# Optimization experiments

Hardware: AMD Instinct MI355X
Metric: run time of the kernel (lower is better)

The kernel has to match this reference:

```python
import jax, jax.numpy as jnp
import numpy as np

DIM = 512
HEADS = 8        # MultiHeadAttention default heads=8 (init 'heads' arg actually sets dim_head)
DIM_HEAD = 64    # from AttentionLayers heads=64 passed positionally as dim_head
HIDDEN = HEADS * DIM_HEAD  # 512
EPS = 1e-5


def setup_inputs() -> dict:
    key = jax.random.key(0)
    ks = jax.random.split(key, 8)
    s = 1.0 / np.sqrt(DIM)
    return {
        "x": jax.random.normal(ks[0], (4, 2048, DIM), dtype=jnp.float32),
        "ln_g": jnp.ones((DIM,), dtype=jnp.float32),
        "ln_b": jnp.zeros((DIM,), dtype=jnp.float32),
        "Wq": jax.random.normal(ks[1], (DIM, HIDDEN), dtype=jnp.float32) * s,
        "Wk": jax.random.normal(ks[2], (DIM, HIDDEN), dtype=jnp.float32) * s,
        "Wv": jax.random.normal(ks[3], (DIM, HIDDEN), dtype=jnp.float32) * s,
        "Wo": jax.random.normal(ks[4], (HIDDEN, DIM), dtype=jnp.float32) * s,
        "bo": jnp.zeros((DIM,), dtype=jnp.float32),
    }


def reference(x, ln_g, ln_b, Wq, Wk, Wv, Wo, bo):
    b, n, d = x.shape
    residual = x
    # pre-norm LayerNorm
    mu = jnp.mean(x, axis=-1, keepdims=True)
    var = jnp.mean((x - mu) ** 2, axis=-1, keepdims=True)
    xn = (x - mu) * jax.lax.rsqrt(var + EPS) * ln_g + ln_b
    # QKV projections (no bias), split into heads: [b, s, h, dh]
    q = (xn @ Wq).reshape(b, n, HEADS, DIM_HEAD)
    k = (xn @ Wk).reshape(b, n, HEADS, DIM_HEAD)
    v = (xn @ Wv).reshape(b, n, HEADS, DIM_HEAD)
    scale = HIDDEN ** (-0.5)  # note: scales by hidden_dim, not dim_head (faithful)
    scores = jnp.einsum('bihd,bjhd->bhij', q, k) * scale  # [b,h,i,j] full matrix
    attn = jax.nn.softmax(scores, axis=-1)
    out = jnp.einsum('bhij,bjhd->bihd', attn, v).reshape(b, n, HIDDEN)
    out = out @ Wo + bo
    # residual; the subsequent FFN layer's output is discarded in the source
    return out + residual
```

## Files before the change

kernel.cpp:

```cpp
#include <hip/hip_runtime.h>
#include <hip/hip_bf16.h>

#define DIM 512
#define SEQ 2048
#define BATCH 4
#define NHEADS 8
#define DH 64
#define NROWS (BATCH * SEQ)
#define LN_EPS 1e-5f

typedef __hip_bfloat16 bf16;
typedef __attribute__((ext_vector_type(8))) short short8;
typedef __attribute__((ext_vector_type(4))) float f32x4;
typedef __attribute__((ext_vector_type(16))) float f32x16;

#define MFMA16(a, b, c) __builtin_amdgcn_mfma_f32_16x16x32_bf16((a), (b), (c), 0, 0, 0)
#define MFMA32(a, b, c) __builtin_amdgcn_mfma_f32_32x32x16_bf16((a), (b), (c), 0, 0, 0)

#if __has_builtin(__builtin_amdgcn_exp2f)
#define EXP2(x) __builtin_amdgcn_exp2f(x)
#else
#define EXP2(x) exp2f(x)
#endif

#if defined(__has_builtin)
#if __has_builtin(__builtin_amdgcn_global_load_lds)
#define HAS_GLDS 1
#endif
#endif

__device__ __forceinline__ void glds16(const bf16* g, bf16* l) {
#ifdef HAS_GLDS
  __builtin_amdgcn_global_load_lds((const __attribute__((address_space(1))) void*)g,
                                   (__attribute__((address_space(3))) void*)l, 16, 0, 0);
#else
  *reinterpret_cast<uint4*>(l) = *reinterpret_cast<const uint4*>(g);
#endif
}

__device__ __forceinline__ void store_bf16x4(bf16* p, float a, float b, float c, float d) {
  bf16 tmp[4] = {__float2bfloat16(a), __float2bfloat16(b), __float2bfloat16(c),
                 __float2bfloat16(d)};
  *reinterpret_cast<ushort4*>(p) = *reinterpret_cast<const ushort4*>(tmp);
}

__device__ __forceinline__ unsigned pk2(float a, float b) {
  union { bf16 h[2]; unsigned u; } x;
  x.h[0] = __float2bfloat16(a);
  x.h[1] = __float2bfloat16(b);
  return x.u;
}

__device__ __forceinline__ short8 mk8(unsigned a, unsigned b, unsigned c, unsigned d) {
  union { unsigned u[4]; short8 s; } x;
  x.u[0] = a; x.u[1] = b; x.u[2] = c; x.u[3] = d;
  return x.s;
}

#define B2F(us) __uint_as_float(((unsigned)(us)) << 16)

#define BARRIER() asm volatile("s_barrier" ::: "memory")
#define WAITVM0() asm volatile("s_waitcnt vmcnt(0)" ::: "memory")

#define Q_SCALE_LOG2E 0.06375872f

__global__ void setup_kernel(const float* __restrict__ x, const float* __restrict__ gamma,
                             const float* __restrict__ beta, bf16* __restrict__ xn,
                             const float* __restrict__ Wq, const float* __restrict__ Wk,
                             const float* __restrict__ Wv, const float* __restrict__ Wo,
                             bf16* __restrict__ Wt) {
  const int t = threadIdx.x;
  if (blockIdx.x < NROWS / 4) {
    const int row = blockIdx.x * 4 + (t >> 6);
    const int l = t & 63;
    const float4* xr = reinterpret_cast<const float4*>(x + (size_t)row * DIM);
    const float4 v0 = xr[l * 2];
    const float4 v1 = xr[l * 2 + 1];
    float s = (v0.x + v0.y + v0.z + v0.w) + (v1.x + v1.y + v1.z + v1.w);
    float ss = v0.x * v0.x + v0.y * v0.y + v0.z * v0.z + v0.w * v0.w + v1.x * v1.x +
               v1.y * v1.y + v1.z * v1.z + v1.w * v1.w;
#pragma unroll
    for (int off = 1; off < 64; off <<= 1) {
      s += __shfl_xor(s, off);
      ss += __shfl_xor(ss, off);
    }
    const float mu = s * (1.0f / DIM);
    const float rs = rsqrtf(ss * (1.0f / DIM) - mu * mu + LN_EPS);
    const float4 g0 = reinterpret_cast<const float4*>(gamma)[l * 2];
    const float4 g1 = reinterpret_cast<const float4*>(gamma)[l * 2 + 1];
    const float4 b0 = reinterpret_cast<const float4*>(beta)[l * 2];
    const float4 b1 = reinterpret_cast<const float4*>(beta)[l * 2 + 1];
    bf16* o = xn + (size_t)row * DIM + l * 8;
    store_bf16x4(o, (v0.x - mu) * rs * g0.x + b0.x, (v0.y - mu) * rs * g0.y + b0.y,
                 (v0.z - mu) * rs * g0.z + b0.z, (v0.w - mu) * rs * g0.w + b0.w);
    store_bf16x4(o + 4, (v1.x - mu) * rs * g1.x + b1.x, (v1.y - mu) * rs * g1.y + b1.y,
                 (v1.z - mu) * rs * g1.z + b1.z, (v1.w - mu) * rs * g1.w + b1.w);
  } else {
    __shared__ float tile[32][33];
    const int idx = blockIdx.x - NROWS / 4;
    const int bx = idx & 15, by = (idx >> 4) & 15, z = idx >> 8;
    const float* __restrict__ W = (z == 0) ? Wq : (z == 1) ? Wk : (z == 2) ? Wv : Wo;
    const float scale = (z == 0) ? Q_SCALE_LOG2E : 1.0f;
    bf16* __restrict__ dst = Wt + (size_t)z * DIM * DIM;
    const int tx = t & 31, ty = t >> 5;
#pragma unroll
    for (int i = 0; i < 32; i += 8)
      tile[ty + i][tx] = W[(size_t)(by * 32 + ty + i) * DIM + bx * 32 + tx];
    __syncthreads();
#pragma unroll
    for (int i = 0; i < 32; i += 8)
      dst[(size_t)(bx * 32 + ty + i) * DIM + by * 32 + tx] =
          __float2bfloat16(tile[tx][ty + i] * scale);
  }
}

__launch_bounds__(256, 3)
__global__ void gemm_qkv_kernel(const bf16* __restrict__ A, const bf16* __restrict__ Bt,
                                bf16* __restrict__ qo, bf16* __restrict__ ko,
                                bf16* __restrict__ vto) {
  const int m0 = blockIdx.x * 128, n0g = blockIdx.y * 128;
  __shared__ __align__(16) char smem[128 * 136 * 2];
  bf16* const sA = (bf16*)smem;
  bf16* const sB = (bf16*)(smem + 16384);
  bf16* const sT = (bf16*)smem;
  const int t = threadIdx.x, w = t >> 6, l = t & 63;
  const int r = l & 15, g = l >> 4;
  const int wm = w >> 1, wn = w & 1;
  const int crow = w * 32 + (l >> 2);
  const int ccol = (l & 3) * 8;
  const bf16* gA = A + (size_t)(m0 + crow) * DIM + ccol;
  const bf16* gB = Bt + (size_t)(n0g + crow) * DIM + ccol;
  const int loff = w * 1024 + l * 8;
  f32x4 acc[4][4] = {};
  glds16(gA, sA + loff);
  glds16(gA + 16 * DIM, sA + loff + 512);
  glds16(gB, sB + loff);
  glds16(gB + 16 * DIM, sB + loff + 512);
  const int NK = DIM / 32;
  for (int ks = 0; ks < NK; ks++) {
    const int cur = ks & 1;
    __syncthreads();
    if (ks + 1 < NK) {
      const int k0n = (ks + 1) * 32;
      glds16(gA + k0n, sA + (1 - cur) * 4096 + loff);
      glds16(gA + 16 * DIM + k0n, sA + (1 - cur) * 4096 + loff + 512);
      glds16(gB + k0n, sB + (1 - cur) * 4096 + loff);
      glds16(gB + 16 * DIM + k0n, sB + (1 - cur) * 4096 + loff + 512);
    }
    short8 af[4], bfv[4];
#pragma unroll
    for (int i = 0; i < 4; i++)
      af[i] = *reinterpret_cast<const short8*>(
          &sA[cur * 4096 + (wm * 64 + i * 16 + r) * 32 + g * 8]);
#pragma unroll
    for (int j = 0; j < 4; j++)
      bfv[j] = *reinterpret_cast<const short8*>(
          &sB[cur * 4096 + (wn * 64 + j * 16 + r) * 32 + g * 8]);
#pragma unroll
    for (int i = 0; i < 4; i++)
#pragma unroll
      for (int j = 0; j < 4; j++) acc[i][j] = MFMA16(af[i], bfv[j], acc[i][j]);
  }
  const int z = n0g >> 9;
  const int b = m0 / SEQ;
  if (z != 2) {
    bf16* __restrict__ outp = (z == 0) ? qo : ko;
    const int nc0 = (n0g & 511) + wn * 64;
#pragma unroll
    for (int i = 0; i < 4; i++)
#pragma unroll
      for (int j = 0; j < 4; j++)
#pragma unroll
        for (int reg = 0; reg < 4; reg++) {
          const int m = m0 + wm * 64 + i * 16 + g * 4 + reg;
          const int col = nc0 + j * 16 + r;
          outp[(size_t)m * DIM + col] = __float2bfloat16(acc[i][j][reg]);
        }
  } else {
    __syncthreads();
#pragma unroll
    for (int i = 0; i < 4; i++)
#pragma unroll
      for (int j = 0; j < 4; j++)
        store_bf16x4(&sT[(wn * 64 + j * 16 + r) * 136 + wm * 64 + i * 16 + g * 4],
                     acc[i][j][0], acc[i][j][1], acc[i][j][2], acc[i][j][3]);
    __syncthreads();
    const int dr = t >> 1;
    const int mc = (t & 1) * 64;
    const int dcol = (n0g & 511) + dr;
    bf16* dst = vto + ((size_t)b * DIM + dcol) * SEQ + (m0 - b * SEQ) + mc;
#pragma unroll
    for (int uu = 0; uu < 8; uu++)
      *reinterpret_cast<uint4*>(dst + uu * 8) =
          *reinterpret_cast<const uint4*>(&sT[dr * 136 + mc + uu * 8]);
  }
}

template <bool SPLIT>
__launch_bounds__(256, 2)
__global__ void attn_kernel(const bf16* __restrict__ q, const bf16* __restrict__ k,
                            const bf16* __restrict__ vt, bf16* __restrict__ opart,
                            float* __restrict__ lpart) {
  const int bh = blockIdx.x, jh = blockIdx.y, it = blockIdx.z;
  const int b = bh >> 3, h = bh & 7;
  const int t = threadIdx.x, wv = t >> 6, l = t & 63;
  const int c2 = l & 31, h2 = l >> 5;
  __shared__ __align__(16) bf16 sK[2][64 * 64];
  __shared__ __align__(16) bf16 sV[2][64 * 64];
  const int i0w = it * 256 + wv * 64;
  const int jbase = SPLIT ? jh * (SEQ / 2) : 0;

  const int srow8 = l >> 3;
  const int u = ((l & 7) - srow8) & 7;
  const bf16* kg = k + ((size_t)(b * SEQ) + jbase + wv * 16 + srow8) * DIM + h * DH + u * 8;
  const bf16* vg = vt + ((size_t)(b * DIM) + h * DH + wv * 16 + srow8) * SEQ + jbase + u * 8;
  const int loff = wv * 1024 + l * 8;
#pragma unroll
  for (int cc = 0; cc < 2; cc++) {
    glds16(kg + (size_t)(cc * 8) * DIM, &sK[0][loff + cc * 512]);
    glds16(vg + (size_t)(cc * 8) * SEQ, &sV[0][loff + cc * 512]);
  }

  const bf16* qp = q + ((size_t)(b * SEQ) + i0w + c2) * DIM + h * DH + h2 * 8;
  short8 qf[2][4];
#pragma unroll
  for (int x = 0; x < 2; x++)
#pragma unroll
    for (int kk = 0; kk < 4; kk++)
      qf[x][kk] = *reinterpret_cast<const short8*>(qp + x * 32 * DIM + kk * 16);

  int eo[4];
#pragma unroll
  for (int x = 0; x < 4; x++) eo[x] = c2 * 64 + 8 * ((2 * x + h2 + c2) & 7);

  f32x16 oacc[2][2] = {};
  float lsum[2] = {0.f, 0.f};
  const int NJ = SPLIT ? (SEQ / 2) / 64 : SEQ / 64;

  for (int jt = 0; jt < NJ; jt++) {
    WAITVM0();
    BARRIER();
    if (jt + 1 < NJ) {
      const int j0n = (jt + 1) * 64;
      const int bn = (jt + 1) & 1;
#pragma unroll
      for (int cc = 0; cc < 2; cc++) {
        glds16(kg + (size_t)(j0n + cc * 8) * DIM, &sK[bn][loff + cc * 512]);
        glds16(vg + (size_t)(cc * 8) * SEQ + j0n, &sV[bn][loff + cc * 512]);
      }
    }
    const bf16* sKb = sK[jt & 1];
    const bf16* sVb = sV[jt & 1];
#pragma unroll
    for (int jb = 0; jb < 2; jb++) {
      short8 kf[4];
#pragma unroll
      for (int kk = 0; kk < 4; kk++)
        kf[kk] = *reinterpret_cast<const short8*>(sKb + jb * 2048 + eo[kk]);
      f32x16 st[2] = {};
#pragma unroll
      for (int kk = 0; kk < 4; kk++) {
        st[0] = MFMA32(kf[kk], qf[0][kk], st[0]);
        st[1] = MFMA32(kf[kk], qf[1][kk], st[1]);
      }
      short8 pf[2][2];
#pragma unroll
      for (int x = 0; x < 2; x++) {
        float p[16];
#pragma unroll
        for (int e = 0; e < 16; e++) p[e] = EXP2(st[x][e]);
        lsum[x] += ((((p[0] + p[1]) + (p[2] + p[3])) + ((p[4] + p[5]) + (p[6] + p[7]))) +
                    (((p[8] + p[9]) + (p[10] + p[11])) + ((p[12] + p[13]) + (p[14] + p[15]))));
        unsigned W[4][2];
#pragma unroll
        for (int a = 0; a < 4; a++)
#pragma unroll
          for (int w = 0; w < 2; w++) W[a][w] = pk2(p[4 * a + 2 * w], p[4 * a + 2 * w + 1]);
#pragma unroll
        for (int k2 = 0; k2 < 2; k2++) {
          unsigned F0, F1, F2, F3;
          {
            const unsigned We = W[2 * k2][0], Wo = W[2 * k2 + 1][0];
            const unsigned te = __shfl_xor(We, 32), to = __shfl_xor(Wo, 32);
            F0 = h2 ? to : We;
            F2 = h2 ? Wo : te;
          }
          {
            const unsigned We = W[2 * k2][1], Wo = W[2 * k2 + 1][1];
            const unsigned te = __shfl_xor(We, 32), to = __shfl_xor(Wo, 32);
            F1 = h2 ? to : We;
            F3 = h2 ? Wo : te;
          }
          pf[x][k2] = mk8(F0, F1, F2, F3);
        }
      }
#pragma unroll
      for (int j2 = 0; j2 < 2; j2++) {
#pragma unroll
        for (int db = 0; db < 2; db++) {
          const short8 vf =
              *reinterpret_cast<const short8*>(sVb + db * 2048 + eo[2 * jb + j2]);
          oacc[0][db] = MFMA32(vf, pf[0][j2], oacc[0][db]);
          oacc[1][db] = MFMA32(vf, pf[1][j2], oacc[1][db]);
        }
      }
    }
  }
  const size_t obase = ((size_t)(SPLIT ? jh * 32 : 0) + bh) * SEQ;
#pragma unroll
  for (int x = 0; x < 2; x++) {
    lsum[x] += __shfl_xor(lsum[x], 32);
    const int i = i0w + x * 32 + c2;
    if (l < 32) lpart[obase + i] = lsum[x];
#pragma unroll
    for (int db = 0; db < 2; db++)
#pragma unroll
      for (int rr = 0; rr < 4; rr++)
        store_bf16x4(opart + (obase + i) * 64 + db * 32 + rr * 8 + h2 * 4,
                     oacc[x][db][4 * rr + 0], oacc[x][db][4 * rr + 1],
                     oacc[x][db][4 * rr + 2], oacc[x][db][4 * rr + 3]);
  }
  if (!SPLIT) {
    const size_t obase1 = ((size_t)32 + bh) * SEQ;
#pragma unroll
    for (int x = 0; x < 2; x++) {
      const int i = i0w + x * 32 + c2;
      if (l < 32) lpart[obase1 + i] = 0.f;
#pragma unroll
      for (int db = 0; db < 2; db++)
#pragma unroll
        for (int rr = 0; rr < 4; rr++)
          store_bf16x4(opart + (obase1 + i) * 64 + db * 32 + rr * 8 + h2 * 4, 0.f, 0.f, 0.f,
                       0.f);
    }
  }
}

__launch_bounds__(256, 2)
__global__ void gemm_proj_kernel(const bf16* __restrict__ opart, const float* __restrict__ lpart,
                                 const bf16* __restrict__ Bt, const float* __restrict__ bo,
                                 const float* __restrict__ x, float* __restrict__ out) {
  const int m0 = blockIdx.x * 128, n0 = blockIdx.y * 64;
  __shared__ __align__(16) bf16 sA[128 * 32];
  __shared__ __align__(16) bf16 sB[64 * 32];
  const int t = threadIdx.x, w = t >> 6, l = t & 63;
  const int r = l & 15, g = l >> 4;
  const int wm = w >> 1, wn = w & 1;
  const int arow = t >> 2;
  const int acol = (t & 3) * 8;
  const bf16* gB = Bt + (size_t)(n0 + arow) * DIM + acol;
  f32x4 acc[4][2] = {};
  const int NK = DIM / 32;
  for (int ks = 0; ks < NK; ks++) {
    const int k0 = ks * 32;
    const int h = k0 >> 6;
    const int d0 = (k0 & 63) + acol;
    uint4 areg[2];
#pragma unroll
    for (int c = 0; c < 2; c++) {
      const int m = m0 + c * 64 + arow;
      const int bb = m >> 11, ii = m & 2047;
      const size_t row0 = ((size_t)(bb * 8 + h)) * SEQ + ii;
      const size_t row1 = row0 + (size_t)32 * SEQ;
      const uint4 A0 = *reinterpret_cast<const uint4*>(opart + row0 * 64 + d0);
      const uint4 A1 = *reinterpret_cast<const uint4*>(opart + row1 * 64 + d0);
      const float inv = 1.0f / (lpart[row0] + lpart[row1]);
      const ushort* a0 = (const ushort*)&A0;
      const ushort* a1 = (const ushort*)&A1;
      bf16 rr[8];
#pragma unroll
      for (int e = 0; e < 8; e++)
        rr[e] = __float2bfloat16((B2F(a0[e]) + B2F(a1[e])) * inv);
      areg[c] = *reinterpret_cast<const uint4*>(rr);
    }
    const uint4 breg = *reinterpret_cast<const uint4*>(gB + k0);
    __syncthreads();
    *reinterpret_cast<uint4*>(&sA[(0 * 64 + arow) * 32 + acol]) = areg[0];
    *reinterpret_cast<uint4*>(&sA[(1 * 64 + arow) * 32 + acol]) = areg[1];
    *reinterpret_cast<uint4*>(&sB[arow * 32 + acol]) = breg;
    __syncthreads();
    short8 af[4], bfv[2];
#pragma unroll
    for (int i = 0; i < 4; i++)
      af[i] = *reinterpret_cast<const short8*>(&sA[(wm * 64 + i * 16 + r) * 32 + g * 8]);
#pragma unroll
    for (int j = 0; j < 2; j++)
      bfv[j] = *reinterpret_cast<const short8*>(&sB[(wn * 32 + j * 16 + r) * 32 + g * 8]);
#pragma unroll
    for (int i = 0; i < 4; i++)
#pragma unroll
      for (int j = 0; j < 2; j++) acc[i][j] = MFMA16(af[i], bfv[j], acc[i][j]);
  }
#pragma unroll
  for (int i = 0; i < 4; i++)
#pragma unroll
    for (int j = 0; j < 2; j++)
#pragma unroll
      for (int reg = 0; reg < 4; reg++) {
        const int m = m0 + wm * 64 + i * 16 + g * 4 + reg;
        const int col = n0 + wn * 32 + j * 16 + r;
        out[(size_t)m * DIM + col] = acc[i][j][reg] + bo[col] + x[(size_t)m * DIM + col];
      }
}

extern "C" void kernel_launch(void* const* d_in, const int* in_sizes, int n_in,
                              void* d_out, int out_size, void* d_ws, size_t ws_size,
                              hipStream_t stream) {
  (void)in_sizes; (void)n_in; (void)out_size;
  const float* x    = (const float*)d_in[0];
  const float* ln_g = (const float*)d_in[1];
  const float* ln_b = (const float*)d_in[2];
  const float* Wq   = (const float*)d_in[3];
  const float* Wk   = (const float*)d_in[4];
  const float* Wv   = (const float*)d_in[5];
  const float* Wo   = (const float*)d_in[6];
  const float* bo   = (const float*)d_in[7];
  float* out = (float*)d_out;
  char* ws = (char*)d_ws;
  bf16* xn  = (bf16*)(ws);
  bf16* wt  = (bf16*)(ws + (8u << 20));
  bf16* qb  = (bf16*)(ws + (10u << 20));
  bf16* kb  = (bf16*)(ws + (18u << 20));
  bf16* vtb = (bf16*)(ws + (26u << 20));
  bf16* opart = (bf16*)(ws + (34u << 20));
  float* lpart = (float*)(ws + (50u << 20));
  const bool split = ws_size >= ((50u << 20) + (1u << 19));

  setup_kernel<<<NROWS / 4 + 1024, 256, 0, stream>>>(x, ln_g, ln_b, xn, Wq, Wk, Wv, Wo, wt);
  gemm_qkv_kernel<<<dim3(NROWS / 128, (3 * DIM) / 128), 256, 0, stream>>>(xn, wt, qb, kb, vtb);
  if (split) {
    attn_kernel<true><<<dim3(BATCH * NHEADS, 2, SEQ / 256), 256, 0, stream>>>(
        qb, kb, vtb, opart, lpart);
  } else {
    attn_kernel<false><<<dim3(BATCH * NHEADS, 1, SEQ / 256), 256, 0, stream>>>(
        qb, kb, vtb, opart, lpart);
  }
  gemm_proj_kernel<<<dim3(NROWS / 128, DIM / 64), 256, 0, stream>>>(
      opart, lpart, wt + 3 * DIM * DIM, bo, x, out);
}
```

Before: 170.0 us.

## Halve per-wave query rows in attention to double blocks and occupancy

The attention kernel now gives each wave 32 query rows instead of 64, so a block covers 128 rows and the grid doubles along the sequence. The register footprint drops (one score tile, half the accumulators), and launch bounds are raised to 4 blocks per SIMD to match. The intent is more parallelism and better latency hiding. The cost is that every K/V tile loaded into LDS is reused by half as many query rows, which doubles K/V global and LDS traffic.

```diff
diff --git a/kernel.cpp b/kernel.cpp
--- a/kernel.cpp
+++ b/kernel.cpp
@@ -197,7 +197,7 @@
 }
 
 template <bool SPLIT>
-__launch_bounds__(256, 2)
+__launch_bounds__(256, 4)
 __global__ void attn_kernel(const bf16* __restrict__ q, const bf16* __restrict__ k,
                             const bf16* __restrict__ vt, bf16* __restrict__ opart,
                             float* __restrict__ lpart) {
@@ -207,7 +207,7 @@
   const int c2 = l & 31, h2 = l >> 5;
   __shared__ __align__(16) bf16 sK[2][64 * 64];
   __shared__ __align__(16) bf16 sV[2][64 * 64];
-  const int i0w = it * 256 + wv * 64;
+  const int i0w = it * 128 + wv * 32;
   const int jbase = SPLIT ? jh * (SEQ / 2) : 0;
 
   const int srow8 = l >> 3;
@@ -222,19 +222,17 @@
   }
 
   const bf16* qp = q + ((size_t)(b * SEQ) + i0w + c2) * DIM + h * DH + h2 * 8;
-  short8 qf[2][4];
-#pragma unroll
-  for (int x = 0; x < 2; x++)
-#pragma unroll
-    for (int kk = 0; kk < 4; kk++)
-      qf[x][kk] = *reinterpret_cast<const short8*>(qp + x * 32 * DIM + kk * 16);
+  short8 qf[4];
+#pragma unroll
+  for (int kk = 0; kk < 4; kk++)
+    qf[kk] = *reinterpret_cast<const short8*>(qp + kk * 16);
 
   int eo[4];
 #pragma unroll
   for (int x = 0; x < 4; x++) eo[x] = c2 * 64 + 8 * ((2 * x + h2 + c2) & 7);
 
-  f32x16 oacc[2][2] = {};
-  float lsum[2] = {0.f, 0.f};
+  f32x16 oacc[2] = {};
+  float lsum = 0.f;
   const int NJ = SPLIT ? (SEQ / 2) / 64 : SEQ / 64;
 
   for (int jt = 0; jt < NJ; jt++) {
@@ -257,42 +255,36 @@
 #pragma unroll
       for (int kk = 0; kk < 4; kk++)
         kf[kk] = *reinterpret_cast<const short8*>(sKb + jb * 2048 + eo[kk]);
-      f32x16 st[2] = {};
-#pragma unroll
-      for (int kk = 0; kk < 4; kk++) {
-        st[0] = MFMA32(kf[kk], qf[0][kk], st[0]);
-        st[1] = MFMA32(kf[kk], qf[1][kk], st[1]);
-      }
-      short8 pf[2][2];
-#pragma unroll
-      for (int x = 0; x < 2; x++) {
-        float p[16];
-#pragma unroll
-        for (int e = 0; e < 16; e++) p[e] = EXP2(st[x][e]);
-        lsum[x] += ((((p[0] + p[1]) + (p[2] + p[3])) + ((p[4] + p[5]) + (p[6] + p[7]))) +
-                    (((p[8] + p[9]) + (p[10] + p[11])) + ((p[12] + p[13]) + (p[14] + p[15]))));
-        unsigned W[4][2];
-#pragma unroll
-        for (int a = 0; a < 4; a++)
-#pragma unroll
-          for (int w = 0; w < 2; w++) W[a][w] = pk2(p[4 * a + 2 * w], p[4 * a + 2 * w + 1]);
-#pragma unroll
-        for (int k2 = 0; k2 < 2; k2++) {
-          unsigned F0, F1, F2, F3;
-          {
-            const unsigned We = W[2 * k2][0], Wo = W[2 * k2 + 1][0];
-            const unsigned te = __shfl_xor(We, 32), to = __shfl_xor(Wo, 32);
-            F0 = h2 ? to : We;
-            F2 = h2 ? Wo : te;
-          }
-          {
-            const unsigned We = W[2 * k2][1], Wo = W[2 * k2 + 1][1];
-            const unsigned te = __shfl_xor(We, 32), to = __shfl_xor(Wo, 32);
-            F1 = h2 ? to : We;
-            F3 = h2 ? Wo : te;
-          }
-          pf[x][k2] = mk8(F0, F1, F2, F3);
+      f32x16 st = {};
+#pragma unroll
+      for (int kk = 0; kk < 4; kk++) st = MFMA32(kf[kk], qf[kk], st);
+      float p[16];
+#pragma unroll
+      for (int e = 0; e < 16; e++) p[e] = EXP2(st[e]);
+      lsum += ((((p[0] + p[1]) + (p[2] + p[3])) + ((p[4] + p[5]) + (p[6] + p[7]))) +
+               (((p[8] + p[9]) + (p[10] + p[11])) + ((p[12] + p[13]) + (p[14] + p[15]))));
+      unsigned W[4][2];
+#pragma unroll
+      for (int a = 0; a < 4; a++)
+#pragma unroll
+        for (int w = 0; w < 2; w++) W[a][w] = pk2(p[4 * a + 2 * w], p[4 * a + 2 * w + 1]);
+      short8 pf[2];
+#pragma unroll
+      for (int k2 = 0; k2 < 2; k2++) {
+        unsigned F0, F1, F2, F3;
+        {
+          const unsigned We = W[2 * k2][0], Wo = W[2 * k2 + 1][0];
+          const unsigned te = __shfl_xor(We, 32), to = __shfl_xor(Wo, 32);
+          F0 = h2 ? to : We;
+          F2 = h2 ? Wo : te;
         }
+        {
+          const unsigned We = W[2 * k2][1], Wo = W[2 * k2 + 1][1];
+          const unsigned te = __shfl_xor(We, 32), to = __shfl_xor(Wo, 32);
+          F1 = h2 ? to : We;
+          F3 = h2 ? Wo : te;
+        }
+        pf[k2] = mk8(F0, F1, F2, F3);
       }
 #pragma unroll
       for (int j2 = 0; j2 < 2; j2++) {
@@ -300,39 +292,31 @@
         for (int db = 0; db < 2; db++) {
           const short8 vf =
               *reinterpret_cast<const short8*>(sVb + db * 2048 + eo[2 * jb + j2]);
-          oacc[0][db] = MFMA32(vf, pf[0][j2], oacc[0][db]);
-          oacc[1][db] = MFMA32(vf, pf[1][j2], oacc[1][db]);
+          oacc[db] = MFMA32(vf, pf[j2], oacc[db]);
         }
       }
     }
   }
   const size_t obase = ((size_t)(SPLIT ? jh * 32 : 0) + bh) * SEQ;
-#pragma unroll
-  for (int x = 0; x < 2; x++) {
-    lsum[x] += __shfl_xor(lsum[x], 32);
-    const int i = i0w + x * 32 + c2;
-    if (l < 32) lpart[obase + i] = lsum[x];
-#pragma unroll
-    for (int db = 0; db < 2; db++)
-#pragma unroll
-      for (int rr = 0; rr < 4; rr++)
-        store_bf16x4(opart + (obase + i) * 64 + db * 32 + rr * 8 + h2 * 4,
-                     oacc[x][db][4 * rr + 0], oacc[x][db][4 * rr + 1],
-                     oacc[x][db][4 * rr + 2], oacc[x][db][4 * rr + 3]);
-  }
+  lsum += __shfl_xor(lsum, 32);
+  const int i = i0w + c2;
+  if (l < 32) lpart[obase + i] = lsum;
+#pragma unroll
+  for (int db = 0; db < 2; db++)
+#pragma unroll
+    for (int rr = 0; rr < 4; rr++)
+      store_bf16x4(opart + (obase + i) * 64 + db * 32 + rr * 8 + h2 * 4,
+                   oacc[db][4 * rr + 0], oacc[db][4 * rr + 1], oacc[db][4 * rr + 2],
+                   oacc[db][4 * rr + 3]);
   if (!SPLIT) {
     const size_t obase1 = ((size_t)32 + bh) * SEQ;
-#pragma unroll
-    for (int x = 0; x < 2; x++) {
-      const int i = i0w + x * 32 + c2;
-      if (l < 32) lpart[obase1 + i] = 0.f;
-#pragma unroll
-      for (int db = 0; db < 2; db++)
-#pragma unroll
-        for (int rr = 0; rr < 4; rr++)
-          store_bf16x4(opart + (obase1 + i) * 64 + db * 32 + rr * 8 + h2 * 4, 0.f, 0.f, 0.f,
-                       0.f);
-    }
+    if (l < 32) lpart[obase1 + i] = 0.f;
+#pragma unroll
+    for (int db = 0; db < 2; db++)
+#pragma unroll
+      for (int rr = 0; rr < 4; rr++)
+        store_bf16x4(opart + (obase1 + i) * 64 + db * 32 + rr * 8 + h2 * 4, 0.f, 0.f, 0.f,
+                     0.f);
   }
 }
 
@@ -429,10 +413,10 @@
   setup_kernel<<<NROWS / 4 + 1024, 256, 0, stream>>>(x, ln_g, ln_b, xn, Wq, Wk, Wv, Wo, wt);
   gemm_qkv_kernel<<<dim3(NROWS / 128, (3 * DIM) / 128), 256, 0, stream>>>(xn, wt, qb, kb, vtb);
   if (split) {
-    attn_kernel<true><<<dim3(BATCH * NHEADS, 2, SEQ / 256), 256, 0, stream>>>(
+    attn_kernel<true><<<dim3(BATCH * NHEADS, 2, SEQ / 128), 256, 0, stream>>>(
         qb, kb, vtb, opart, lpart);
   } else {
-    attn_kernel<false><<<dim3(BATCH * NHEADS, 1, SEQ / 256), 256, 0, stream>>>(
+    attn_kernel<false><<<dim3(BATCH * NHEADS, 1, SEQ / 128), 256, 0, stream>>>(
         qb, kb, vtb, opart, lpart);
   }
   gemm_proj_kernel<<<dim3(NROWS / 128, DIM / 64), 256, 0, stream>>>(
```

Measured after the change: 169.7 us. Within noise of the previous version (-0.2%).
